# Optimization experiments

Measured on AMD Instinct MI355X. Metric: run time of the kernel, lower is better.

The kernel has to match this reference:

```python
import jax, jax.numpy as jnp
import numpy as np

N_NODES = 100000
N_EDGES = 3200000
IN_DIM = 256
HIDDEN = 128
OUT_DIM = 64


def setup_inputs() -> dict:
    key = jax.random.key(0)
    k = jax.random.split(key, 6)
    x = jax.random.normal(k[0], (N_NODES, IN_DIM), dtype=jnp.float32)
    adj_vals = jax.random.uniform(k[1], (N_EDGES,), dtype=jnp.float32)
    # glorot init as in the original
    s1 = np.sqrt(6.0 / (IN_DIM + HIDDEN)).astype(np.float32)
    s2 = np.sqrt(6.0 / (HIDDEN + OUT_DIM)).astype(np.float32)
    w1 = jax.random.uniform(k[2], (IN_DIM, HIDDEN), dtype=jnp.float32, minval=-s1, maxval=s1)
    w2 = jax.random.uniform(k[3], (HIDDEN, OUT_DIM), dtype=jnp.float32, minval=-s2, maxval=s2)
    edge_src = jax.random.randint(k[4], (N_EDGES,), 0, N_NODES, dtype=jnp.int32)
    edge_dst = jax.random.randint(k[5], (N_EDGES,), 0, N_NODES, dtype=jnp.int32)
    return {"x": x, "adj_vals": adj_vals, "w1": w1, "w2": w2,
            "edge_src": edge_src, "edge_dst": edge_dst}


def _spmm(adj_vals, edge_src, edge_dst, h, n_nodes):
    """Sparse adjacency (COO) times dense matrix: out[d] = sum_e vals[e]*h[src[e]]."""
    msgs = adj_vals[:, None] * h[edge_src]  # [E, D] gather + scale
    return jax.ops.segment_sum(msgs, edge_dst, num_segments=n_nodes)


def reference(x, adj_vals, w1, w2, edge_src, edge_dst):
    # Layer 1: pre_sup = X @ W1; support = A @ pre_sup; relu
    h = jax.nn.relu(_spmm(adj_vals, edge_src, edge_dst, x @ w1, N_NODES))
    # Layer 2: identity activation -> logits
    logits = _spmm(adj_vals, edge_src, edge_dst, h @ w2, N_NODES)
    return logits
```

## Files before the change

kernel.cpp:

```cpp
#include <hip/hip_runtime.h>

#define N_NODES 100000
#define N_EDGES 3200000
#define IN_DIM 256
#define HIDDEN 128
#define OUT_DIM 64

#define NBUCK 782
#define CHUNK 5120
#define BCAP 6144

typedef unsigned int uint32;
typedef unsigned short ushort16;

typedef short short8 __attribute__((ext_vector_type(8)));
typedef float f32x4 __attribute__((ext_vector_type(4)));

__device__ __forceinline__ ushort16 f2bf(float f) {
    uint32 u = __float_as_uint(f);
    u += 0x7fffu + ((u >> 16) & 1u);
    return (ushort16)(u >> 16);
}

__device__ __forceinline__ void splitbf(float f, unsigned short& hi, unsigned short& lo) {
    uint32 u = __float_as_uint(f);
    uint32 r = u + 0x7fffu + ((u >> 16) & 1u);
    hi = (unsigned short)(r >> 16);
    float hf = __uint_as_float((r >> 16) << 16);
    float res = f - hf;
    uint32 v = __float_as_uint(res);
    lo = (unsigned short)((v + 0x7fffu + ((v >> 16) & 1u)) >> 16);
}


__global__ __launch_bounds__(256)
void hist_bucket(const int* __restrict__ edst, int* __restrict__ bcnt, int E) {
    __shared__ int h[NBUCK];
    for (int b = threadIdx.x; b < NBUCK; b += 256) h[b] = 0;
    __syncthreads();
    for (int i = blockIdx.x * 256 + threadIdx.x; i < E; i += gridDim.x * 256)
        atomicAdd(&h[edst[i] >> 7], 1);
    __syncthreads();
    for (int b = threadIdx.x; b < NBUCK; b += 256) {
        int c = h[b];
        if (c) atomicAdd(&bcnt[b], c);
    }
}


__global__ __launch_bounds__(256)
void bucket_scan(const int* __restrict__ bcnt, int* __restrict__ bptr,
                 int* __restrict__ cursor, int* __restrict__ row_ptr, int E) {
    __shared__ int st[256];
    int tid = threadIdx.x;
    int v4[4];
    int s0 = 0;
#pragma unroll
    for (int k = 0; k < 4; k++) {
        int b = tid * 4 + k;
        v4[k] = (b < NBUCK) ? bcnt[b] : 0;
        s0 += v4[k];
    }
    st[tid] = s0;
    __syncthreads();
    for (int off = 1; off < 256; off <<= 1) {
        int t = (tid >= off) ? st[tid - off] : 0;
        __syncthreads();
        st[tid] += t;
        __syncthreads();
    }
    int run = st[tid] - s0;
#pragma unroll
    for (int k = 0; k < 4; k++) {
        int b = tid * 4 + k;
        if (b < NBUCK) { bptr[b] = run; cursor[b] = run; }
        run += v4[k];
    }
    if (tid == 255) bptr[NBUCK] = run;
    if (tid == 0) row_ptr[N_NODES] = E;
}


__global__ __launch_bounds__(256)
void partition_kernel(const int* __restrict__ esrc, const int* __restrict__ edst,
                      const float* __restrict__ evals, int* __restrict__ cursor,
                      int2* __restrict__ part, int E) {
    __shared__ int hist[NBUCK];
    __shared__ int basepos[NBUCK];
    __shared__ int st[256];
    __shared__ unsigned short sbb[CHUNK];
    __shared__ int2 sbp[CHUNK];
    int tid = threadIdx.x;
    long base = (long)blockIdx.x * CHUNK;
    int cnt = (int)min((long)CHUNK, (long)E - base);

    for (int b = tid; b < NBUCK; b += 256) hist[b] = 0;
    __syncthreads();
    for (int j = tid; j < cnt; j += 256)
        atomicAdd(&hist[edst[base + j] >> 7], 1);
    __syncthreads();

    int v4[4];
    int s0 = 0;
#pragma unroll
    for (int k = 0; k < 4; k++) {
        int b = tid * 4 + k;
        v4[k] = (b < NBUCK) ? hist[b] : 0;
        s0 += v4[k];
    }
    st[tid] = s0;
    __syncthreads();
    for (int off = 1; off < 256; off <<= 1) {
        int t = (tid >= off) ? st[tid - off] : 0;
        __syncthreads();
        st[tid] += t;
        __syncthreads();
    }
    int run = st[tid] - s0;
#pragma unroll
    for (int k = 0; k < 4; k++) {
        int b = tid * 4 + k;
        if (b < NBUCK) {
            int gbase = (v4[k] > 0) ? atomicAdd(&cursor[b], v4[k]) : 0;
            basepos[b] = gbase - run;
            hist[b] = run;
        }
        run += v4[k];
    }
    __syncthreads();

    for (int j = tid; j < cnt; j += 256) {
        int d = edst[base + j];
        int b = d >> 7;
        int pos = atomicAdd(&hist[b], 1);
        sbb[pos] = (unsigned short)b;
        sbp[pos] = make_int2(esrc[base + j] | ((d & 127) << 17),
                             __float_as_int(evals[base + j]));
    }
    __syncthreads();

    for (int j = tid; j < cnt; j += 256) {
        int b = sbb[j];
        part[basepos[b] + j] = sbp[j];
    }
}


__global__ __launch_bounds__(256)
void bucket_to_csr(const int* __restrict__ bptr, int2* __restrict__ part,
                   int* __restrict__ row_ptr) {
    __shared__ int2 se[BCAP];
    __shared__ int rcnt[128];
    __shared__ int rcur[128];
    int tid = threadIdx.x;
    int b = blockIdx.x;
    int s = bptr[b], e = bptr[b + 1];
    int cnt = min(e - s, BCAP);

    if (tid < 128) rcnt[tid] = 0;
    __syncthreads();
    for (int j = tid; j < cnt; j += 256) {
        int2 p = part[s + j];
        se[j] = p;
        atomicAdd(&rcnt[p.x >> 17], 1);
    }
    __syncthreads();

    int v = (tid < 128) ? rcnt[tid] : 0;
    if (tid < 128) rcur[tid] = v;
    __syncthreads();
    for (int off = 1; off < 128; off <<= 1) {
        int t = 0;
        if (tid < 128 && tid >= off) t = rcur[tid - off];
        __syncthreads();
        if (tid < 128 && tid >= off) rcur[tid] += t;
        __syncthreads();
    }
    if (tid < 128) {
        int excl = rcur[tid] - v;
        rcur[tid] = excl;
        int row = b * 128 + tid;
        if (row < N_NODES) row_ptr[row] = s + excl;
    }
    __syncthreads();

    for (int j = tid; j < cnt; j += 256) {
        int2 p = se[j];
        int r = p.x >> 17;
        int pos = atomicAdd(&rcur[r], 1);
        part[s + pos] = make_int2(p.x & 0x1FFFF, p.y);
    }
}


__global__ __launch_bounds__(256)
void splitw_kernel(const float* __restrict__ w1, const float* __restrict__ w2,
                   unsigned short* __restrict__ w1f_hi, unsigned short* __restrict__ w1f_lo,
                   unsigned short* __restrict__ w2f_hi, unsigned short* __restrict__ w2f_lo) {
    const int W1_SLOTS = (IN_DIM / 32) * (HIDDEN / 16) * 64;
    const int W2_SLOTS = (HIDDEN / 32) * (OUT_DIM / 16) * 64;
    int g = blockIdx.x * 256 + threadIdx.x;
    if (g < W1_SLOTS) {
        int lane = g & 63;
        int rest = g >> 6;
        int nfrag = rest & 7;
        int kblk = rest >> 3;
        int n = nfrag * 16 + (lane & 15);
        int k0 = kblk * 32 + (lane >> 4) * 8;
#pragma unroll
        for (int j = 0; j < 8; j++) {
            unsigned short h, l;
            splitbf(w1[(size_t)(k0 + j) * HIDDEN + n], h, l);
            w1f_hi[(size_t)g * 8 + j] = h;
            w1f_lo[(size_t)g * 8 + j] = l;
        }
    } else if (g < W1_SLOTS + W2_SLOTS) {
        int g2 = g - W1_SLOTS;
        int lane = g2 & 63;
        int rest = g2 >> 6;
        int nfrag = rest & 3;
        int kblk = rest >> 2;
        int n = nfrag * 16 + (lane & 15);
        int k0 = kblk * 32 + (lane >> 4) * 8;
#pragma unroll
        for (int j = 0; j < 8; j++) {
            unsigned short h, l;
            splitbf(w2[(size_t)(k0 + j) * OUT_DIM + n], h, l);
            w2f_hi[(size_t)g2 * 8 + j] = h;
            w2f_lo[(size_t)g2 * 8 + j] = l;
        }
    }
}


template <int K, int BN>
__launch_bounds__(256)
__global__ void gemm_mfma(const float* __restrict__ A,
                          const unsigned short* __restrict__ Bf_hi,
                          const unsigned short* __restrict__ Bf_lo,
                          ushort16* __restrict__ C, int M) {
    constexpr int BM = 128, BK = 64;
    constexpr int NF = BN / 32;
    __shared__ __align__(16) unsigned short Ah[BM * BK];
    __shared__ __align__(16) unsigned short Al[BM * BK];

    int tid = threadIdx.x;
    int wid = tid >> 6, lane = tid & 63;
    int wr = wid >> 1, wc = wid & 1;
    int rowBase = blockIdx.x * BM;
    int r = lane & 15, kg = lane >> 4;
    int swzmask = (lane & 7) << 4;

    f32x4 zero = {0.f, 0.f, 0.f, 0.f};
    f32x4 acc[4][NF];
#pragma unroll
    for (int m = 0; m < 4; m++)
#pragma unroll
        for (int n = 0; n < NF; n++) acc[m][n] = zero;

    int sk4 = (tid & 15) * 4;
    int sm0 = tid >> 4;

    for (int k0 = 0; k0 < K; k0 += BK) {
#pragma unroll
        for (int i = 0; i < 8; i++) {
            int m = sm0 + i * 16;
            int row = rowBase + m;
            float4 f = make_float4(0.f, 0.f, 0.f, 0.f);
            if (row < M) f = *(const float4*)(A + (size_t)row * K + k0 + sk4);
            ushort4 h, l;
            splitbf(f.x, h.x, l.x);
            splitbf(f.y, h.y, l.y);
            splitbf(f.z, h.z, l.z);
            splitbf(f.w, h.w, l.w);
            int bo = (m * BK + sk4) * 2;
            int swz = bo ^ ((m & 7) << 4);
            *(ushort4*)((char*)Ah + swz) = h;
            *(ushort4*)((char*)Al + swz) = l;
        }
        __syncthreads();

#pragma unroll
        for (int kk = 0; kk < BK / 32; kk++) {
            short8 ah[4], al[4];
            int abase = (wr * 64 + r) * (BK * 2) + kk * 64 + kg * 16;
#pragma unroll
            for (int m = 0; m < 4; m++) {
                int swz = (abase + m * (16 * BK * 2)) ^ swzmask;
                ah[m] = *(const short8*)((const char*)Ah + swz);
                al[m] = *(const short8*)((const char*)Al + swz);
            }
            short8 bh[NF], bl[NF];
            int kblk = (k0 >> 5) + kk;
#pragma unroll
            for (int n = 0; n < NF; n++) {
                int nf = wc * NF + n;
                size_t off = ((size_t)(kblk * (BN / 16) + nf) * 64 + lane) * 8;
                bh[n] = *(const short8*)(Bf_hi + off);
                bl[n] = *(const short8*)(Bf_lo + off);
            }
#pragma unroll
            for (int m = 0; m < 4; m++)
#pragma unroll
                for (int n = 0; n < NF; n++) {
                    acc[m][n] = __builtin_amdgcn_mfma_f32_16x16x32_bf16(ah[m], bh[n], acc[m][n], 0, 0, 0);
                    acc[m][n] = __builtin_amdgcn_mfma_f32_16x16x32_bf16(ah[m], bl[n], acc[m][n], 0, 0, 0);
                    acc[m][n] = __builtin_amdgcn_mfma_f32_16x16x32_bf16(al[m], bh[n], acc[m][n], 0, 0, 0);
                }
        }
        __syncthreads();
    }

#pragma unroll
    for (int m = 0; m < 4; m++) {
        int row0 = rowBase + wr * 64 + m * 16 + kg * 4;
#pragma unroll
        for (int j = 0; j < 4; j++) {
            int row = row0 + j;
            if (row < M) {
#pragma unroll
                for (int n = 0; n < NF; n++) {
                    int col = wc * (BN / 2) + n * 16 + r;
                    C[(size_t)row * BN + col] = f2bf(acc[m][n][j]);
                }
            }
        }
    }
}


template <int D, bool RELU>
__launch_bounds__(256)
__global__ void spmm_kernel(const ushort16* __restrict__ feat, const int2* __restrict__ csr_pair,
                            const int* __restrict__ row_ptr, float* __restrict__ out, int n) {
    constexpr int LPR = D * 2 / 16;
    constexpr int EPG = 64 / LPR;
    int wid = threadIdx.x >> 6;
    int lane = threadIdx.x & 63;
    int row = blockIdx.x * 4 + wid;
    if (row >= n) return;
    int s = row_ptr[row], e = row_ptr[row + 1];

    int sub = lane / LPR;
    int slot = lane % LPR;
    const char* fbase = (const char*)feat + slot * 16;

    float acc[8];
#pragma unroll
    for (int j = 0; j < 8; j++) acc[j] = 0.f;

    for (int i = s; i < e; i += 4 * EPG) {
        int2 p[4]; float v[4]; uint4 u[4];
#pragma unroll
        for (int q = 0; q < 4; q++) {
            int ii = i + q * EPG + sub;
            p[q] = csr_pair[min(ii, e - 1)];
            v[q] = (ii < e) ? __int_as_float(p[q].y) : 0.f;
        }
#pragma unroll
        for (int q = 0; q < 4; q++)
            u[q] = *(const uint4*)(fbase + (size_t)p[q].x * (D * 2));
#pragma unroll
        for (int q = 0; q < 4; q++) {
#pragma unroll
            for (int t = 0; t < 4; t++) {
                uint32 w = (&u[q].x)[t];
                acc[2 * t]     += v[q] * __uint_as_float(w << 16);
                acc[2 * t + 1] += v[q] * __uint_as_float(w & 0xffff0000u);
            }
        }
    }

#pragma unroll
    for (int m = LPR; m < 64; m <<= 1) {
#pragma unroll
        for (int j = 0; j < 8; j++) acc[j] += __shfl_xor(acc[j], m);
    }

    if (RELU) {
#pragma unroll
        for (int j = 0; j < 8; j++) acc[j] = acc[j] > 0.f ? acc[j] : 0.f;
    }

    if (lane < LPR) {
        float4* o = (float4*)(out + (size_t)row * D + slot * 8);
        o[0] = make_float4(acc[0], acc[1], acc[2], acc[3]);
        o[1] = make_float4(acc[4], acc[5], acc[6], acc[7]);
    }
}


extern "C" void kernel_launch(void* const* d_in, const int* in_sizes, int n_in,
                              void* d_out, int out_size, void* d_ws, size_t ws_size,
                              hipStream_t stream) {
    const float* x    = (const float*)d_in[0];
    const float* adj  = (const float*)d_in[1];
    const float* w1   = (const float*)d_in[2];
    const float* w2   = (const float*)d_in[3];
    const int*   esrc = (const int*)d_in[4];
    const int*   edst = (const int*)d_in[5];
    float* out = (float*)d_out;

    const int N = N_NODES;
    const int E = N_EDGES;

    char* ws = (char*)d_ws;
    size_t off = 0;
    auto take = [&](size_t bytes) -> char* {
        char* p = ws + off;
        off = (off + bytes + 255) & ~(size_t)255;
        return p;
    };
    int*      bcnt    = (int*)take((size_t)NBUCK * 4);
    int*      bptr    = (int*)take((size_t)(NBUCK + 1) * 4);
    int*      cursor  = (int*)take((size_t)NBUCK * 4);
    int*      row_ptr = (int*)take((size_t)(N + 1) * 4);
    int2*     part    = (int2*)take((size_t)E * 8);
    ushort16* pre1    = (ushort16*)take((size_t)N * HIDDEN * 2);
    ushort16* pre2    = (ushort16*)take((size_t)N * OUT_DIM * 2);
    float*    h       = (float*)take((size_t)N * HIDDEN * 4);
    unsigned short* w1f_hi = (unsigned short*)take((size_t)HIDDEN * IN_DIM * 2);
    unsigned short* w1f_lo = (unsigned short*)take((size_t)HIDDEN * IN_DIM * 2);
    unsigned short* w2f_hi = (unsigned short*)take((size_t)OUT_DIM * HIDDEN * 2);
    unsigned short* w2f_lo = (unsigned short*)take((size_t)OUT_DIM * HIDDEN * 2);

    splitw_kernel<<<20, 256, 0, stream>>>(w1, w2, w1f_hi, w1f_lo, w2f_hi, w2f_lo);

    hipMemsetAsync(bcnt, 0, (size_t)NBUCK * 4, stream);
    hist_bucket<<<1024, 256, 0, stream>>>(edst, bcnt, E);
    bucket_scan<<<1, 256, 0, stream>>>(bcnt, bptr, cursor, row_ptr, E);
    partition_kernel<<<(E + CHUNK - 1) / CHUNK, 256, 0, stream>>>(esrc, edst, adj, cursor, part, E);
    bucket_to_csr<<<NBUCK, 256, 0, stream>>>(bptr, part, row_ptr);

    gemm_mfma<IN_DIM, HIDDEN><<<(N + 127) / 128, 256, 0, stream>>>(x, w1f_hi, w1f_lo, pre1, N);
    spmm_kernel<HIDDEN, true><<<(N + 3) / 4, 256, 0, stream>>>(pre1, part, row_ptr, h, N);

    gemm_mfma<HIDDEN, OUT_DIM><<<(N + 127) / 128, 256, 0, stream>>>(h, w2f_hi, w2f_lo, pre2, N);
    spmm_kernel<OUT_DIM, false><<<(N + 3) / 4, 256, 0, stream>>>(pre2, part, row_ptr, out, N);
}
```

Baseline: 549.0 us.

## Simplify edge partition: drop local sort, pad global cursors, halve chunk size

```diff
diff --git a/kernel.cpp b/kernel.cpp
--- a/kernel.cpp
+++ b/kernel.cpp
@@ -7,8 +7,10 @@
 #define OUT_DIM 64
 
 #define NBUCK 782
-#define CHUNK 5120
+#define CHUNK 2560
+#define NPT (CHUNK / 256)
 #define BCAP 6144
+#define CURSTRIDE 32
 
 typedef unsigned int uint32;
 typedef unsigned short ushort16;
@@ -73,7 +75,7 @@
 #pragma unroll
     for (int k = 0; k < 4; k++) {
         int b = tid * 4 + k;
-        if (b < NBUCK) { bptr[b] = run; cursor[b] = run; }
+        if (b < NBUCK) { bptr[b] = run; cursor[b * CURSTRIDE] = run; }
         run += v4[k];
     }
     if (tid == 255) bptr[NBUCK] = run;
@@ -86,62 +88,42 @@
                       const float* __restrict__ evals, int* __restrict__ cursor,
                       int2* __restrict__ part, int E) {
     __shared__ int hist[NBUCK];
-    __shared__ int basepos[NBUCK];
-    __shared__ int st[256];
-    __shared__ unsigned short sbb[CHUNK];
-    __shared__ int2 sbp[CHUNK];
+    __shared__ int base_[NBUCK];
     int tid = threadIdx.x;
     long base = (long)blockIdx.x * CHUNK;
     int cnt = (int)min((long)CHUNK, (long)E - base);
 
     for (int b = tid; b < NBUCK; b += 256) hist[b] = 0;
     __syncthreads();
-    for (int j = tid; j < cnt; j += 256)
-        atomicAdd(&hist[edst[base + j] >> 7], 1);
-    __syncthreads();
-
-    int v4[4];
-    int s0 = 0;
-#pragma unroll
-    for (int k = 0; k < 4; k++) {
-        int b = tid * 4 + k;
-        v4[k] = (b < NBUCK) ? hist[b] : 0;
-        s0 += v4[k];
-    }
-    st[tid] = s0;
-    __syncthreads();
-    for (int off = 1; off < 256; off <<= 1) {
-        int t = (tid >= off) ? st[tid - off] : 0;
-        __syncthreads();
-        st[tid] += t;
-        __syncthreads();
-    }
-    int run = st[tid] - s0;
-#pragma unroll
-    for (int k = 0; k < 4; k++) {
-        int b = tid * 4 + k;
-        if (b < NBUCK) {
-            int gbase = (v4[k] > 0) ? atomicAdd(&cursor[b], v4[k]) : 0;
-            basepos[b] = gbase - run;
-            hist[b] = run;
-        }
-        run += v4[k];
-    }
-    __syncthreads();
-
-    for (int j = tid; j < cnt; j += 256) {
-        int d = edst[base + j];
-        int b = d >> 7;
-        int pos = atomicAdd(&hist[b], 1);
-        sbb[pos] = (unsigned short)b;
-        sbp[pos] = make_int2(esrc[base + j] | ((d & 127) << 17),
-                             __float_as_int(evals[base + j]));
-    }
-    __syncthreads();
-
-    for (int j = tid; j < cnt; j += 256) {
-        int b = sbb[j];
-        part[basepos[b] + j] = sbp[j];
+
+    int d[NPT];
+#pragma unroll
+    for (int k = 0; k < NPT; k++) {
+        int j = tid + k * 256;
+        d[k] = -1;
+        if (j < cnt) {
+            d[k] = edst[base + j];
+            atomicAdd(&hist[d[k] >> 7], 1);
+        }
+    }
+    __syncthreads();
+
+    for (int b = tid; b < NBUCK; b += 256) {
+        int c = hist[b];
+        base_[b] = c ? atomicAdd(&cursor[b * CURSTRIDE], c) : 0;
+        hist[b] = 0;
+    }
+    __syncthreads();
+
+#pragma unroll
+    for (int k = 0; k < NPT; k++) {
+        int j = tid + k * 256;
+        if (j < cnt) {
+            int dd = d[k], b = dd >> 7;
+            int off2 = atomicAdd(&hist[b], 1);
+            part[base_[b] + off2] = make_int2(esrc[base + j] | ((dd & 127) << 17),
+                                              __float_as_int(evals[base + j]));
+        }
     }
 }
 
@@ -413,7 +395,7 @@
     };
     int*      bcnt    = (int*)take((size_t)NBUCK * 4);
     int*      bptr    = (int*)take((size_t)(NBUCK + 1) * 4);
-    int*      cursor  = (int*)take((size_t)NBUCK * 4);
+    int*      cursor  = (int*)take((size_t)NBUCK * CURSTRIDE * 4);
     int*      row_ptr = (int*)take((size_t)(N + 1) * 4);
     int2*     part    = (int2*)take((size_t)E * 8);
     ushort16* pre1    = (ushort16*)take((size_t)N * HIDDEN * 2);
```

Measured after the change: 547.7 us. Within noise of the previous version (-0.2%).
